# Optimization experiments

Hardware: AMD Instinct MI355X
Metric: run time of the kernel (lower is better)

Reference implementation:

```python
import jax, jax.numpy as jnp
import numpy as np
import math

N, M_KV = 8192, 8192
QDIM, KDIM, MID = 256, 256, 128
NEG_BIG = -float(1 << 32)  # matches torch.masked_fill(Attn, mask, -(1 << 32))


def setup_inputs() -> dict:
    key = jax.random.key(0)
    ks = jax.random.split(key, 8)
    main_feat = jax.random.normal(ks[0], (N, QDIM), dtype=jnp.float32)
    other_feat = jax.random.normal(ks[1], (M_KV, KDIM), dtype=jnp.float32)
    fix_feat = jax.random.uniform(ks[2], (M_KV,), dtype=jnp.float32)
    mask = jax.random.randint(ks[3], (N, M_KV), 0, 2).astype(jnp.bool_)
    # Linear params (torch.nn.Linear stores weight as [out, in])
    Wq = jax.random.normal(ks[4], (MID, QDIM), dtype=jnp.float32) / math.sqrt(QDIM)
    bq = jax.random.normal(ks[5], (MID,), dtype=jnp.float32) * 0.01
    Wk = jax.random.normal(ks[6], (MID, KDIM), dtype=jnp.float32) / math.sqrt(KDIM)
    bk = jax.random.normal(ks[7], (MID,), dtype=jnp.float32) * 0.01
    return {"main_feat": main_feat, "other_feat": other_feat, "fix_feat": fix_feat,
            "mask": mask, "Wq": Wq, "bq": bq, "Wk": Wk, "bk": bk}


def reference(main_feat, other_feat, fix_feat, mask, Wq, bq, Wk, bk):
    # Projections: y = x @ W.T + b
    Q = main_feat @ Wq.T + bq            # [N, MID]
    K = other_feat @ Wk.T + bk           # [M, MID]
    scale = 1.0 / math.sqrt(MID)
    attn = jnp.einsum('nd,md->nm', Q, K) * scale   # [N, M]
    attn = jnp.where(mask, NEG_BIG, attn)
    attn = jax.nn.softmax(attn, axis=-1)
    # diag(fix_feat) @ other_feat is just a row-wise scale of V
    V = fix_feat[:, None] * other_feat   # [M, KDIM]
    return attn @ V                      # [N, KDIM]
```

## Files before the change

kernel.cpp:

```cpp
#include <hip/hip_runtime.h>
#include <hip/hip_bf16.h>
#include <stdint.h>

typedef __attribute__((ext_vector_type(8))) short short8;
typedef __attribute__((ext_vector_type(4))) float floatx4;

#define MFMA32K(a, b, c) __builtin_amdgcn_mfma_f32_16x16x32_bf16(a, b, c, 0, 0, 0)

constexpr int N_Q  = 8192;
constexpr int M_KV = 8192;
constexpr int DMID = 128;
constexpr int DV   = 256;

__device__ __forceinline__ unsigned short f2bf(float x) {
    unsigned u = __float_as_uint(x);
    u += 0x7fffu + ((u >> 16) & 1u);
    return (unsigned short)(u >> 16);
}

__device__ __forceinline__ short8 cvt_f8_bf8(float4 a, float4 b) {
    short8 r;
    r[0] = (short)f2bf(a.x); r[1] = (short)f2bf(a.y);
    r[2] = (short)f2bf(a.z); r[3] = (short)f2bf(a.w);
    r[4] = (short)f2bf(b.x); r[5] = (short)f2bf(b.y);
    r[6] = (short)f2bf(b.z); r[7] = (short)f2bf(b.w);
    return r;
}

__device__ __forceinline__ void gl_lds16(const unsigned short* g, unsigned short* l) {
    __builtin_amdgcn_global_load_lds(
        (const __attribute__((address_space(1))) unsigned int*)g,
        (__attribute__((address_space(3))) unsigned int*)l, 16, 0, 0);
}

__device__ __forceinline__ unsigned nz4(unsigned x) {
    unsigned nz = (((x & 0x7f7f7f7fu) + 0x7f7f7f7fu) | x) & 0x80808080u;
    unsigned a = (nz >> 7) & 0x01010101u;
    return (a * 0x01020408u) >> 24;
}

__global__ __launch_bounds__(256) void proj_kernel(
    const float* __restrict__ main_feat, const float* __restrict__ Wq, const float* __restrict__ bq,
    const float* __restrict__ other_feat, const float* __restrict__ Wk, const float* __restrict__ bk,
    unsigned short* __restrict__ Qw, unsigned short* __restrict__ Kw)
{
    const float* src;  const float* W;  const float* bias;  unsigned short* dst;
    if (blockIdx.y == 0) { src = main_feat;  W = Wq; bias = bq; dst = Qw; }
    else                 { src = other_feat; W = Wk; bias = bk; dst = Kw; }

    const int wave = threadIdx.x >> 6, lane = threadIdx.x & 63;
    const int n = lane & 15, quad = lane >> 4;
    const int row0 = blockIdx.x * 64 + wave * 16;

    short8 a[8];
    const float* ap = src + (size_t)(row0 + n) * 256 + quad * 8;
#pragma unroll
    for (int ks = 0; ks < 8; ++ks) {
        float4 x0 = *(const float4*)(ap + ks * 32);
        float4 x1 = *(const float4*)(ap + ks * 32 + 4);
        a[ks] = cvt_f8_bf8(x0, x1);
    }

    floatx4 acc[8];
#pragma unroll
    for (int nt = 0; nt < 8; ++nt) acc[nt] = floatx4{0.f, 0.f, 0.f, 0.f};

#pragma unroll
    for (int nt = 0; nt < 8; ++nt) {
        const float* wp = W + (size_t)(nt * 16 + n) * 256 + quad * 8;
#pragma unroll
        for (int ks = 0; ks < 8; ++ks) {
            float4 w0 = *(const float4*)(wp + ks * 32);
            float4 w1 = *(const float4*)(wp + ks * 32 + 4);
            short8 b = cvt_f8_bf8(w0, w1);
            acc[nt] = MFMA32K(a[ks], b, acc[nt]);
        }
    }

#pragma unroll
    for (int nt = 0; nt < 8; ++nt) {
        float bb = bias[nt * 16 + n];
#pragma unroll
        for (int reg = 0; reg < 4; ++reg) {
            int r = row0 + quad * 4 + reg;
            int c = nt * 16 + n;
            int phys = ((((c >> 3) + r) & 15) << 3) | (c & 7);
            dst[(size_t)r * DMID + phys] = f2bf(acc[nt][reg] + bb);
        }
    }
}

__global__ __launch_bounds__(256) void build_vt_kernel(
    const float* __restrict__ other_feat, const float* __restrict__ fix_feat,
    unsigned short* __restrict__ Vt)
{
    __shared__ unsigned short tile[64 * 72];
    const int t = threadIdx.x;
    const int m0 = blockIdx.x * 64, d0 = blockIdx.y * 64;

#pragma unroll
    for (int r = 0; r < 4; ++r) {
        int idx = r * 256 + t;
        int ml = idx >> 4, dl4 = (idx & 15) * 4;
        float4 v = *(const float4*)(other_feat + (size_t)(m0 + ml) * 256 + d0 + dl4);
        float f = fix_feat[m0 + ml];
        tile[(dl4 + 0) * 72 + ml] = f2bf(v.x * f);
        tile[(dl4 + 1) * 72 + ml] = f2bf(v.y * f);
        tile[(dl4 + 2) * 72 + ml] = f2bf(v.z * f);
        tile[(dl4 + 3) * 72 + ml] = f2bf(v.w * f);
    }
    __syncthreads();
#pragma unroll
    for (int r = 0; r < 8; ++r) {
        int dl = r * 8 + (t >> 5);
        int d = d0 + dl;
        int ml = (t & 31) * 2;
        int e = ml >> 5, s = (ml >> 4) & 1, q = (ml >> 2) & 3, j = ml & 3;
        int pc = e * 32 + q * 8 + s * 4 + j;
        int phys = ((((pc >> 3) + d) & 7) << 3) | (pc & 7);
        unsigned int v0 = tile[dl * 72 + ml];
        unsigned int v1 = tile[dl * 72 + ml + 1];
        *(unsigned int*)(Vt + (size_t)d * M_KV + m0 + phys) = v0 | (v1 << 16);
    }
}

template<int ESZ>
__device__ __forceinline__ void flash_body(
    const unsigned short* __restrict__ Qw, const unsigned short* __restrict__ Kw,
    const unsigned short* __restrict__ Vt, const unsigned int* __restrict__ mask,
    unsigned short* __restrict__ Opart, float* __restrict__ Lpart,
    int nsplit, int lgNs,
    unsigned short* k_lds , unsigned short* vt_lds )
{
    const int L = blockIdx.x + gridDim.x * blockIdx.y;
    const int ly = L & (nsplit - 1);
    const int lx = L >> lgNs;
    const int chunkLen = M_KV >> lgNs;
    const int mBeg = ly * chunkLen;
    const int iters = chunkLen / 64;
    const int phase = lx & (iters - 1);
    const int tid = threadIdx.x;
    const int wave = tid >> 6, lane = tid & 63, n = lane & 15, quad = lane >> 4;
    const int qrow0 = lx * 128 + wave * 32;
    constexpr float SC = 0.08838834764831845f * 1.4426950408889634f;

    auto mcol = [&](int it) {
        int idx = it + phase;
        if (idx >= iters) idx -= iters;
        return mBeg + idx * 64;
    };

    short8 qf[2][4];
#pragma unroll
    for (int qt = 0; qt < 2; ++qt)
#pragma unroll
        for (int db = 0; db < 4; ++db) {
            int row = qrow0 + qt * 16 + n;
            int phys = (db * 4 + quad + row) & 15;
            qf[qt][db] = *(const short8*)(Qw + (size_t)row * DMID + phys * 8);
        }

    floatx4 Oacc[2][16];
#pragma unroll
    for (int qt = 0; qt < 2; ++qt)
#pragma unroll
        for (int dt = 0; dt < 16; ++dt) Oacc[qt][dt] = floatx4{0.f, 0.f, 0.f, 0.f};

    float lrow[2] = {0.f, 0.f};

    const unsigned short* kg = Kw + (size_t)(wave * 4 + (lane >> 4)) * DMID + (lane & 15) * 8;
    const unsigned short* vg = Vt + (size_t)(wave * 8 + (lane >> 3)) * M_KV + (lane & 7) * 8;
    unsigned short* vld = &vt_lds[wave * 512];
    const int kqn = quad + n;

    uint4    mv4[2][4];
    unsigned mv1[2][4];

    auto load_mask = [&](int m0l) {
#pragma unroll
        for (int qt = 0; qt < 2; ++qt) {
            const size_t row = (size_t)(qrow0 + qt * 16 + n);
            if constexpr (ESZ == 4) {
                const unsigned* mp = mask + row * M_KV + m0l + quad * 4;
#pragma unroll
                for (int kvt = 0; kvt < 4; ++kvt)
                    mv4[qt][kvt] = *(const uint4*)(mp + kvt * 16);
            } else {
                const unsigned* mp = mask + row * (M_KV / 4) + (m0l >> 2) + quad;
#pragma unroll
                for (int kvt = 0; kvt < 4; ++kvt)
                    mv1[qt][kvt] = mp[kvt * 4];
            }
        }
    };

    {
        const int m0p = mcol(0);
#pragma unroll
        for (int r = 0; r < 4; ++r)
            gl_lds16(kg + (size_t)(m0p + r * 16) * DMID, &k_lds[wave * 512 + r * 2048]);
        load_mask(m0p);
    }

    for (int it = 0; it < iters; ++it) {
        const int m0 = mcol(it);
        const unsigned short* kbuf = k_lds + (it & 1) * 8192;

        __syncthreads();

#pragma unroll
        for (int r = 0; r < 8; ++r)
            gl_lds16(vg + (size_t)(r * 32) * M_KV + m0, vld + r * 2048);

        unsigned wq[2];
#pragma unroll
        for (int qt = 0; qt < 2; ++qt) {
            unsigned b = 0;
            if constexpr (ESZ == 4) {
#pragma unroll
                for (int kvt = 0; kvt < 4; ++kvt) {
                    const unsigned* c = (const unsigned*)&mv4[qt][kvt];
#pragma unroll
                    for (int j = 0; j < 4; ++j)
                        b |= (c[j] != 0u ? 1u : 0u) << (kvt * 4 + j);
                }
            } else {
#pragma unroll
                for (int kvt = 0; kvt < 4; ++kvt)
                    b |= nz4(mv1[qt][kvt]) << (kvt * 4);
            }
            wq[qt] = b;
        }

        floatx4 ST[4][2];
        __builtin_amdgcn_s_setprio(1);
#pragma unroll
        for (int kvt = 0; kvt < 4; ++kvt) {
            const int rowoff = (kvt * 16 + n) * DMID;
            short8 a0 = *(const short8*)&kbuf[rowoff + (((kqn + 0) & 15) << 3)];
            short8 a1 = *(const short8*)&kbuf[rowoff + (((kqn + 4) & 15) << 3)];
            short8 a2 = *(const short8*)&kbuf[rowoff + (((kqn + 8) & 15) << 3)];
            short8 a3 = *(const short8*)&kbuf[rowoff + (((kqn + 12) & 15) << 3)];
#pragma unroll
            for (int qt = 0; qt < 2; ++qt) {
                floatx4 s = floatx4{0.f, 0.f, 0.f, 0.f};
                s = MFMA32K(a0, qf[qt][0], s);
                s = MFMA32K(a1, qf[qt][1], s);
                s = MFMA32K(a2, qf[qt][2], s);
                s = MFMA32K(a3, qf[qt][3], s);
                ST[kvt][qt] = s;
            }
        }
        __builtin_amdgcn_s_setprio(0);

        short8 pf8[2][2];
#pragma unroll
        for (int qt = 0; qt < 2; ++qt) {
            const unsigned x = wq[qt];
            float lacc = 0.f;
#pragma unroll
            for (int kvt = 0; kvt < 4; ++kvt) {
                int e = kvt >> 1, s = kvt & 1;
                float p[4];
#pragma unroll
                for (int j = 0; j < 4; ++j) {
                    float v = __builtin_amdgcn_exp2f(ST[kvt][qt][j] * SC);
                    p[j] = ((x >> (kvt * 4 + j)) & 1u) ? 0.f : v;
                    lacc += p[j];
                }
                __hip_bfloat162 h0 = __float22bfloat162_rn(make_float2(p[0], p[1]));
                __hip_bfloat162 h1 = __float22bfloat162_rn(make_float2(p[2], p[3]));
                unsigned u0, u1;
                __builtin_memcpy(&u0, &h0, 4);
                __builtin_memcpy(&u1, &h1, 4);
                ((unsigned*)&pf8[qt][e])[s * 2 + 0] = u0;
                ((unsigned*)&pf8[qt][e])[s * 2 + 1] = u1;
            }
            lrow[qt] += lacc;
        }

        __syncthreads();

        if (it + 1 < iters) {
            const int m1 = mcol(it + 1);
            unsigned short* knext = k_lds + ((it + 1) & 1) * 8192 + wave * 512;
#pragma unroll
            for (int r = 0; r < 4; ++r)
                gl_lds16(kg + (size_t)(m1 + r * 16) * DMID, knext + r * 2048);
            load_mask(m1);
        }

        __builtin_amdgcn_s_setprio(1);
#pragma unroll
        for (int e = 0; e < 2; ++e) {
#pragma unroll
            for (int dt = 0; dt < 16; ++dt) {
                const int vb = (dt * 16 + n) * 64 + (((e * 4 + quad + n) & 7) << 3);
                short8 bv = *(const short8*)&vt_lds[vb];
                Oacc[0][dt] = MFMA32K(pf8[0][e], bv, Oacc[0][dt]);
                Oacc[1][dt] = MFMA32K(pf8[1][e], bv, Oacc[1][dt]);
            }
        }
        __builtin_amdgcn_s_setprio(0);
    }

    const size_t obase = (size_t)ly * N_Q * DV;
#pragma unroll
    for (int qt = 0; qt < 2; ++qt)
#pragma unroll
        for (int dt = 0; dt < 16; ++dt)
#pragma unroll
            for (int reg = 0; reg < 4; ++reg) {
                int gr = qrow0 + qt * 16 + quad * 4 + reg;
                Opart[obase + (size_t)gr * DV + dt * 16 + n] = f2bf(Oacc[qt][dt][reg]);
            }
#pragma unroll
    for (int qt = 0; qt < 2; ++qt) {
        float r = lrow[qt];
        r += __shfl_xor(r, 16);
        r += __shfl_xor(r, 32);
        if (quad == 0)
            Lpart[ly * N_Q + qrow0 + qt * 16 + n] = r;
    }
}

__global__ __launch_bounds__(256, 2) void flash_kernel(
    const unsigned short* __restrict__ Qw, const unsigned short* __restrict__ Kw,
    const unsigned short* __restrict__ Vt, const unsigned int* __restrict__ mask,
    unsigned short* __restrict__ Opart, float* __restrict__ Lpart,
    int nsplit, int lgNs)
{
    __shared__ __align__(16) unsigned short k_lds[2][64 * 128];
    __shared__ __align__(16) unsigned short vt_lds[256 * 64];

    unsigned w0 = mask[threadIdx.x & 63];
    bool isf = (w0 == 0x3f800000u);
    bool isb = (w0 > 1u) && !isf;
    bool wide = (__ballot(isf) != 0ull) || (__ballot(isb) == 0ull);

    if (wide)
        flash_body<4>(Qw, Kw, Vt, mask, Opart, Lpart, nsplit, lgNs,
                      &k_lds[0][0], vt_lds);
    else
        flash_body<1>(Qw, Kw, Vt, mask, Opart, Lpart, nsplit, lgNs,
                      &k_lds[0][0], vt_lds);
}

__global__ __launch_bounds__(256) void combine_kernel(
    const unsigned short* __restrict__ Opart, const float* __restrict__ Lpart,
    float* __restrict__ out, int nsplit)
{
    const int row = blockIdx.x, d = threadIdx.x;
    float L = 0.f, o = 0.f;
    for (int c = 0; c < nsplit; ++c) {
        L += Lpart[c * N_Q + row];
        unsigned int b = Opart[((size_t)c * N_Q + row) * DV + d];
        o += __uint_as_float(b << 16);
    }
    out[(size_t)row * DV + d] = o / L;
}

extern "C" void kernel_launch(void* const* d_in, const int* in_sizes, int n_in,
                              void* d_out, int out_size, void* d_ws, size_t ws_size,
                              hipStream_t stream)
{
    const float* main_feat  = (const float*)d_in[0];
    const float* other_feat = (const float*)d_in[1];
    const float* fix_feat   = (const float*)d_in[2];
    const void*  mask       = d_in[3];
    const float* Wq         = (const float*)d_in[4];
    const float* bq         = (const float*)d_in[5];
    const float* Wk         = (const float*)d_in[6];
    const float* bk         = (const float*)d_in[7];
    float* out = (float*)d_out;

    char* ws = (char*)d_ws;
    unsigned short* Qw = (unsigned short*)(ws);
    unsigned short* Kw = (unsigned short*)(ws + (1ull << 21));
    unsigned short* Vt = (unsigned short*)(ws + (2ull << 21));
    float* Lpart = (float*)(ws + (16ull << 20) + 2048);

    const size_t base = (16ull << 20) + 2048;
    auto need = [&](int ns) {
        return base + (size_t)ns * N_Q * 4 + (size_t)ns * N_Q * DV * 2;
    };
    int nsplit = 1, lgNs = 0;
    if (ws_size >= need(8))      { nsplit = 8; lgNs = 3; }
    else if (ws_size >= need(4)) { nsplit = 4; lgNs = 2; }
    else if (ws_size >= need(2)) { nsplit = 2; lgNs = 1; }

    unsigned short* Opart = (unsigned short*)(Lpart + (size_t)nsplit * N_Q);

    hipLaunchKernelGGL(proj_kernel, dim3(128, 2), dim3(256), 0, stream,
                       main_feat, Wq, bq, other_feat, Wk, bk, Qw, Kw);
    hipLaunchKernelGGL(build_vt_kernel, dim3(128, 4), dim3(256), 0, stream,
                       other_feat, fix_feat, Vt);
    hipLaunchKernelGGL(flash_kernel, dim3(64, nsplit), dim3(256), 0, stream,
                       Qw, Kw, Vt, (const unsigned int*)mask, Opart, Lpart, nsplit, lgNs);
    hipLaunchKernelGGL(combine_kernel, dim3(N_Q), dim3(256), 0, stream,
                       Opart, Lpart, out, nsplit);
}
```

Baseline: 459.9 us.

## Drop LDS staging of K and V; read MFMA operands directly from global memory

Removes the shared-memory double buffer for K and the V tile. Each wave now loads its K and Vt MFMA fragments straight from global memory (through L2/L1), which eliminates both block-wide barriers per iteration and frees LDS. In exchange, every wave in the block redundantly fetches the same K/V data, and the loads are no longer prefetched ahead of the compute, so the MFMAs may stall on global-memory latency.

```diff
diff --git a/kernel.cpp b/kernel.cpp
--- a/kernel.cpp
+++ b/kernel.cpp
@@ -25,12 +25,6 @@
     r[4] = (short)f2bf(b.x); r[5] = (short)f2bf(b.y);
     r[6] = (short)f2bf(b.z); r[7] = (short)f2bf(b.w);
     return r;
-}
-
-__device__ __forceinline__ void gl_lds16(const unsigned short* g, unsigned short* l) {
-    __builtin_amdgcn_global_load_lds(
-        (const __attribute__((address_space(1))) unsigned int*)g,
-        (__attribute__((address_space(3))) unsigned int*)l, 16, 0, 0);
 }
 
 __device__ __forceinline__ unsigned nz4(unsigned x) {
@@ -129,8 +123,7 @@
     const unsigned short* __restrict__ Qw, const unsigned short* __restrict__ Kw,
     const unsigned short* __restrict__ Vt, const unsigned int* __restrict__ mask,
     unsigned short* __restrict__ Opart, float* __restrict__ Lpart,
-    int nsplit, int lgNs,
-    unsigned short* k_lds , unsigned short* vt_lds )
+    int nsplit, int lgNs)
 {
     const int L = blockIdx.x + gridDim.x * blockIdx.y;
     const int ly = L & (nsplit - 1);
@@ -168,9 +161,6 @@
 
     float lrow[2] = {0.f, 0.f};
 
-    const unsigned short* kg = Kw + (size_t)(wave * 4 + (lane >> 4)) * DMID + (lane & 15) * 8;
-    const unsigned short* vg = Vt + (size_t)(wave * 8 + (lane >> 3)) * M_KV + (lane & 7) * 8;
-    unsigned short* vld = &vt_lds[wave * 512];
     const int kqn = quad + n;
 
     uint4    mv4[2][4];
@@ -194,23 +184,10 @@
         }
     };
 
-    {
-        const int m0p = mcol(0);
-#pragma unroll
-        for (int r = 0; r < 4; ++r)
-            gl_lds16(kg + (size_t)(m0p + r * 16) * DMID, &k_lds[wave * 512 + r * 2048]);
-        load_mask(m0p);
-    }
+    load_mask(mcol(0));
 
     for (int it = 0; it < iters; ++it) {
         const int m0 = mcol(it);
-        const unsigned short* kbuf = k_lds + (it & 1) * 8192;
-
-        __syncthreads();
-
-#pragma unroll
-        for (int r = 0; r < 8; ++r)
-            gl_lds16(vg + (size_t)(r * 32) * M_KV + m0, vld + r * 2048);
 
         unsigned wq[2];
 #pragma unroll
@@ -236,11 +213,11 @@
         __builtin_amdgcn_s_setprio(1);
 #pragma unroll
         for (int kvt = 0; kvt < 4; ++kvt) {
-            const int rowoff = (kvt * 16 + n) * DMID;
-            short8 a0 = *(const short8*)&kbuf[rowoff + (((kqn + 0) & 15) << 3)];
-            short8 a1 = *(const short8*)&kbuf[rowoff + (((kqn + 4) & 15) << 3)];
-            short8 a2 = *(const short8*)&kbuf[rowoff + (((kqn + 8) & 15) << 3)];
-            short8 a3 = *(const short8*)&kbuf[rowoff + (((kqn + 12) & 15) << 3)];
+            const unsigned short* krow = Kw + (size_t)(m0 + kvt * 16 + n) * DMID;
+            short8 a0 = *(const short8*)(krow + (((kqn + 0) & 15) << 3));
+            short8 a1 = *(const short8*)(krow + (((kqn + 4) & 15) << 3));
+            short8 a2 = *(const short8*)(krow + (((kqn + 8) & 15) << 3));
+            short8 a3 = *(const short8*)(krow + (((kqn + 12) & 15) << 3));
 #pragma unroll
             for (int qt = 0; qt < 2; ++qt) {
                 floatx4 s = floatx4{0.f, 0.f, 0.f, 0.f};
@@ -279,24 +256,15 @@
             lrow[qt] += lacc;
         }
 
-        __syncthreads();
-
-        if (it + 1 < iters) {
-            const int m1 = mcol(it + 1);
-            unsigned short* knext = k_lds + ((it + 1) & 1) * 8192 + wave * 512;
-#pragma unroll
-            for (int r = 0; r < 4; ++r)
-                gl_lds16(kg + (size_t)(m1 + r * 16) * DMID, knext + r * 2048);
-            load_mask(m1);
-        }
+        if (it + 1 < iters) load_mask(mcol(it + 1));
 
         __builtin_amdgcn_s_setprio(1);
 #pragma unroll
         for (int e = 0; e < 2; ++e) {
 #pragma unroll
             for (int dt = 0; dt < 16; ++dt) {
-                const int vb = (dt * 16 + n) * 64 + (((e * 4 + quad + n) & 7) << 3);
-                short8 bv = *(const short8*)&vt_lds[vb];
+                const unsigned short* vrow = Vt + (size_t)(dt * 16 + n) * M_KV + m0;
+                short8 bv = *(const short8*)(vrow + (((e * 4 + quad + n) & 7) << 3));
                 Oacc[0][dt] = MFMA32K(pf8[0][e], bv, Oacc[0][dt]);
                 Oacc[1][dt] = MFMA32K(pf8[1][e], bv, Oacc[1][dt]);
             }
@@ -330,20 +298,15 @@
     unsigned short* __restrict__ Opart, float* __restrict__ Lpart,
     int nsplit, int lgNs)
 {
-    __shared__ __align__(16) unsigned short k_lds[2][64 * 128];
-    __shared__ __align__(16) unsigned short vt_lds[256 * 64];
-
     unsigned w0 = mask[threadIdx.x & 63];
     bool isf = (w0 == 0x3f800000u);
     bool isb = (w0 > 1u) && !isf;
     bool wide = (__ballot(isf) != 0ull) || (__ballot(isb) == 0ull);
 
     if (wide)
-        flash_body<4>(Qw, Kw, Vt, mask, Opart, Lpart, nsplit, lgNs,
-                      &k_lds[0][0], vt_lds);
+        flash_body<4>(Qw, Kw, Vt, mask, Opart, Lpart, nsplit, lgNs);
     else
-        flash_body<1>(Qw, Kw, Vt, mask, Opart, Lpart, nsplit, lgNs,
-                      &k_lds[0][0], vt_lds);
+        flash_body<1>(Qw, Kw, Vt, mask, Opart, Lpart, nsplit, lgNs);
 }
 
 __global__ __launch_bounds__(256) void combine_kernel(
```

Measured after the change: 621.5 us. 1.35x slower.

## Use 8 waves of 16 query rows each with manual waitcnt/barrier pipelining

Applied to the files above, without the earlier changes.

The flash kernel now runs 512 threads per block, with each wave owning one 16-row query tile instead of two, which halves per-wave accumulators and register pressure. The launch bounds go to (512,4) to target higher occupancy. K, V and mask loads are reissued earlier in each iteration, and __syncthreads is replaced by explicit s_waitcnt vmcnt/lgkmcnt plus s_barrier with sched_barriers, so memory traffic overlaps compute. In exchange each K/V tile in LDS is reused by fewer query rows per wave, the block carries more barrier traffic, and the hand-tuned vmcnt counts must match the number of outstanding loads.

```diff
diff --git a/kernel.cpp b/kernel.cpp
--- a/kernel.cpp
+++ b/kernel.cpp
@@ -141,7 +141,7 @@
     const int phase = lx & (iters - 1);
     const int tid = threadIdx.x;
     const int wave = tid >> 6, lane = tid & 63, n = lane & 15, quad = lane >> 4;
-    const int qrow0 = lx * 128 + wave * 32;
+    const int qrow0 = lx * 128 + wave * 16;
     constexpr float SC = 0.08838834764831845f * 1.4426950408889634f;
 
     auto mcol = [&](int it) {
@@ -150,89 +150,87 @@
         return mBeg + idx * 64;
     };
 
-    short8 qf[2][4];
-#pragma unroll
-    for (int qt = 0; qt < 2; ++qt)
-#pragma unroll
-        for (int db = 0; db < 4; ++db) {
-            int row = qrow0 + qt * 16 + n;
-            int phys = (db * 4 + quad + row) & 15;
-            qf[qt][db] = *(const short8*)(Qw + (size_t)row * DMID + phys * 8);
-        }
-
-    floatx4 Oacc[2][16];
-#pragma unroll
-    for (int qt = 0; qt < 2; ++qt)
-#pragma unroll
-        for (int dt = 0; dt < 16; ++dt) Oacc[qt][dt] = floatx4{0.f, 0.f, 0.f, 0.f};
-
-    float lrow[2] = {0.f, 0.f};
+    short8 qf[4];
+#pragma unroll
+    for (int db = 0; db < 4; ++db) {
+        int row = qrow0 + n;
+        int phys = (db * 4 + quad + row) & 15;
+        qf[db] = *(const short8*)(Qw + (size_t)row * DMID + phys * 8);
+    }
+
+    floatx4 Oacc[16];
+#pragma unroll
+    for (int dt = 0; dt < 16; ++dt) Oacc[dt] = floatx4{0.f, 0.f, 0.f, 0.f};
+
+    float lrow = 0.f;
 
     const unsigned short* kg = Kw + (size_t)(wave * 4 + (lane >> 4)) * DMID + (lane & 15) * 8;
     const unsigned short* vg = Vt + (size_t)(wave * 8 + (lane >> 3)) * M_KV + (lane & 7) * 8;
-    unsigned short* vld = &vt_lds[wave * 512];
     const int kqn = quad + n;
 
-    uint4    mv4[2][4];
-    unsigned mv1[2][4];
+    uint4    mv4[4];
+    unsigned mv1[4];
 
     auto load_mask = [&](int m0l) {
-#pragma unroll
-        for (int qt = 0; qt < 2; ++qt) {
-            const size_t row = (size_t)(qrow0 + qt * 16 + n);
-            if constexpr (ESZ == 4) {
-                const unsigned* mp = mask + row * M_KV + m0l + quad * 4;
-#pragma unroll
-                for (int kvt = 0; kvt < 4; ++kvt)
-                    mv4[qt][kvt] = *(const uint4*)(mp + kvt * 16);
-            } else {
-                const unsigned* mp = mask + row * (M_KV / 4) + (m0l >> 2) + quad;
-#pragma unroll
-                for (int kvt = 0; kvt < 4; ++kvt)
-                    mv1[qt][kvt] = mp[kvt * 4];
-            }
+        const size_t row = (size_t)(qrow0 + n);
+        if constexpr (ESZ == 4) {
+            const unsigned* mp = mask + row * M_KV + m0l + quad * 4;
+#pragma unroll
+            for (int kvt = 0; kvt < 4; ++kvt)
+                mv4[kvt] = *(const uint4*)(mp + kvt * 16);
+        } else {
+            const unsigned* mp = mask + row * (M_KV / 4) + (m0l >> 2) + quad;
+#pragma unroll
+            for (int kvt = 0; kvt < 4; ++kvt)
+                mv1[kvt] = mp[kvt * 4];
         }
     };
 
-    {
-        const int m0p = mcol(0);
-#pragma unroll
-        for (int r = 0; r < 4; ++r)
-            gl_lds16(kg + (size_t)(m0p + r * 16) * DMID, &k_lds[wave * 512 + r * 2048]);
-        load_mask(m0p);
-    }
+#pragma unroll
+    for (int r = 0; r < 2; ++r)
+        gl_lds16(kg + (size_t)(mcol(0) + r * 32) * DMID, &k_lds[wave * 512 + r * 4096]);
+    __builtin_amdgcn_sched_barrier(0);
+    load_mask(mcol(0));
+    __builtin_amdgcn_sched_barrier(0);
+    asm volatile("s_waitcnt vmcnt(4)\n\ts_barrier" ::: "memory");
 
     for (int it = 0; it < iters; ++it) {
         const int m0 = mcol(it);
         const unsigned short* kbuf = k_lds + (it & 1) * 8192;
 
-        __syncthreads();
-
-#pragma unroll
-        for (int r = 0; r < 8; ++r)
-            gl_lds16(vg + (size_t)(r * 32) * M_KV + m0, vld + r * 2048);
-
-        unsigned wq[2];
-#pragma unroll
-        for (int qt = 0; qt < 2; ++qt) {
-            unsigned b = 0;
-            if constexpr (ESZ == 4) {
-#pragma unroll
-                for (int kvt = 0; kvt < 4; ++kvt) {
-                    const unsigned* c = (const unsigned*)&mv4[qt][kvt];
-#pragma unroll
-                    for (int j = 0; j < 4; ++j)
-                        b |= (c[j] != 0u ? 1u : 0u) << (kvt * 4 + j);
-                }
-            } else {
-#pragma unroll
-                for (int kvt = 0; kvt < 4; ++kvt)
-                    b |= nz4(mv1[qt][kvt]) << (kvt * 4);
+#pragma unroll
+        for (int r = 0; r < 4; ++r)
+            gl_lds16(vg + (size_t)(r * 64) * M_KV + m0, &vt_lds[wave * 512 + r * 4096]);
+        const bool more = (it + 1 < iters);
+        if (more) {
+            const int m1 = mcol(it + 1);
+            unsigned short* knext = k_lds + ((it + 1) & 1) * 8192 + wave * 512;
+#pragma unroll
+            for (int r = 0; r < 2; ++r)
+                gl_lds16(kg + (size_t)(m1 + r * 32) * DMID, knext + r * 4096);
+        }
+        __builtin_amdgcn_sched_barrier(0);
+
+        unsigned wq = 0;
+        if constexpr (ESZ == 4) {
+#pragma unroll
+            for (int kvt = 0; kvt < 4; ++kvt) {
+                const unsigned* c = (const unsigned*)&mv4[kvt];
+#pragma unroll
+                for (int j = 0; j < 4; ++j)
+                    wq |= (c[j] != 0u ? 1u : 0u) << (kvt * 4 + j);
             }
-            wq[qt] = b;
-        }
-
-        floatx4 ST[4][2];
+        } else {
+#pragma unroll
+            for (int kvt = 0; kvt < 4; ++kvt)
+                wq |= nz4(mv1[kvt]) << (kvt * 4);
+        }
+        __builtin_amdgcn_sched_barrier(0);
+
+        if (more) load_mask(mcol(it + 1));
+        __builtin_amdgcn_sched_barrier(0);
+
+        floatx4 ST[4];
         __builtin_amdgcn_s_setprio(1);
 #pragma unroll
         for (int kvt = 0; kvt < 4; ++kvt) {
@@ -241,54 +239,39 @@
             short8 a1 = *(const short8*)&kbuf[rowoff + (((kqn + 4) & 15) << 3)];
             short8 a2 = *(const short8*)&kbuf[rowoff + (((kqn + 8) & 15) << 3)];
             short8 a3 = *(const short8*)&kbuf[rowoff + (((kqn + 12) & 15) << 3)];
-#pragma unroll
-            for (int qt = 0; qt < 2; ++qt) {
-                floatx4 s = floatx4{0.f, 0.f, 0.f, 0.f};
-                s = MFMA32K(a0, qf[qt][0], s);
-                s = MFMA32K(a1, qf[qt][1], s);
-                s = MFMA32K(a2, qf[qt][2], s);
-                s = MFMA32K(a3, qf[qt][3], s);
-                ST[kvt][qt] = s;
+            floatx4 s = floatx4{0.f, 0.f, 0.f, 0.f};
+            s = MFMA32K(a0, qf[0], s);
+            s = MFMA32K(a1, qf[1], s);
+            s = MFMA32K(a2, qf[2], s);
+            s = MFMA32K(a3, qf[3], s);
+            ST[kvt] = s;
+        }
+        __builtin_amdgcn_s_setprio(0);
+
+        short8 pf8[2];
+#pragma unroll
+        for (int kvt = 0; kvt < 4; ++kvt) {
+            int e = kvt >> 1, s = kvt & 1;
+            float p[4];
+#pragma unroll
+            for (int j = 0; j < 4; ++j) {
+                float v = __builtin_amdgcn_exp2f(ST[kvt][j] * SC);
+                p[j] = ((wq >> (kvt * 4 + j)) & 1u) ? 0.f : v;
+                lrow += p[j];
             }
-        }
-        __builtin_amdgcn_s_setprio(0);
-
-        short8 pf8[2][2];
-#pragma unroll
-        for (int qt = 0; qt < 2; ++qt) {
-            const unsigned x = wq[qt];
-            float lacc = 0.f;
-#pragma unroll
-            for (int kvt = 0; kvt < 4; ++kvt) {
-                int e = kvt >> 1, s = kvt & 1;
-                float p[4];
-#pragma unroll
-                for (int j = 0; j < 4; ++j) {
-                    float v = __builtin_amdgcn_exp2f(ST[kvt][qt][j] * SC);
-                    p[j] = ((x >> (kvt * 4 + j)) & 1u) ? 0.f : v;
-                    lacc += p[j];
-                }
-                __hip_bfloat162 h0 = __float22bfloat162_rn(make_float2(p[0], p[1]));
-                __hip_bfloat162 h1 = __float22bfloat162_rn(make_float2(p[2], p[3]));
-                unsigned u0, u1;
-                __builtin_memcpy(&u0, &h0, 4);
-                __builtin_memcpy(&u1, &h1, 4);
-                ((unsigned*)&pf8[qt][e])[s * 2 + 0] = u0;
-                ((unsigned*)&pf8[qt][e])[s * 2 + 1] = u1;
-            }
-            lrow[qt] += lacc;
-        }
-
-        __syncthreads();
-
-        if (it + 1 < iters) {
-            const int m1 = mcol(it + 1);
-            unsigned short* knext = k_lds + ((it + 1) & 1) * 8192 + wave * 512;
-#pragma unroll
-            for (int r = 0; r < 4; ++r)
-                gl_lds16(kg + (size_t)(m1 + r * 16) * DMID, knext + r * 2048);
-            load_mask(m1);
-        }
+            __hip_bfloat162 h0 = __float22bfloat162_rn(make_float2(p[0], p[1]));
+            __hip_bfloat162 h1 = __float22bfloat162_rn(make_float2(p[2], p[3]));
+            unsigned u0, u1;
+            __builtin_memcpy(&u0, &h0, 4);
+            __builtin_memcpy(&u1, &h1, 4);
+            ((unsigned*)&pf8[e])[s * 2 + 0] = u0;
+            ((unsigned*)&pf8[e])[s * 2 + 1] = u1;
+        }
+
+        if (more)
+            asm volatile("s_waitcnt vmcnt(4) lgkmcnt(0)\n\ts_barrier" ::: "memory");
+        else
+            asm volatile("s_waitcnt vmcnt(0) lgkmcnt(0)\n\ts_barrier" ::: "memory");
 
         __builtin_amdgcn_s_setprio(1);
 #pragma unroll
@@ -297,34 +280,32 @@
             for (int dt = 0; dt < 16; ++dt) {
                 const int vb = (dt * 16 + n) * 64 + (((e * 4 + quad + n) & 7) << 3);
                 short8 bv = *(const short8*)&vt_lds[vb];
-                Oacc[0][dt] = MFMA32K(pf8[0][e], bv, Oacc[0][dt]);
-                Oacc[1][dt] = MFMA32K(pf8[1][e], bv, Oacc[1][dt]);
+                Oacc[dt] = MFMA32K(pf8[e], bv, Oacc[dt]);
             }
         }
         __builtin_amdgcn_s_setprio(0);
+
+        asm volatile("s_waitcnt lgkmcnt(0)\n\ts_barrier" ::: "memory");
     }
 
     const size_t obase = (size_t)ly * N_Q * DV;
 #pragma unroll
-    for (int qt = 0; qt < 2; ++qt)
-#pragma unroll
-        for (int dt = 0; dt < 16; ++dt)
-#pragma unroll
-            for (int reg = 0; reg < 4; ++reg) {
-                int gr = qrow0 + qt * 16 + quad * 4 + reg;
-                Opart[obase + (size_t)gr * DV + dt * 16 + n] = f2bf(Oacc[qt][dt][reg]);
-            }
-#pragma unroll
-    for (int qt = 0; qt < 2; ++qt) {
-        float r = lrow[qt];
+    for (int dt = 0; dt < 16; ++dt)
+#pragma unroll
+        for (int reg = 0; reg < 4; ++reg) {
+            int gr = qrow0 + quad * 4 + reg;
+            Opart[obase + (size_t)gr * DV + dt * 16 + n] = f2bf(Oacc[dt][reg]);
+        }
+    {
+        float r = lrow;
         r += __shfl_xor(r, 16);
         r += __shfl_xor(r, 32);
         if (quad == 0)
-            Lpart[ly * N_Q + qrow0 + qt * 16 + n] = r;
-    }
-}
-
-__global__ __launch_bounds__(256, 2) void flash_kernel(
+            Lpart[ly * N_Q + qrow0 + n] = r;
+    }
+}
+
+__global__ __launch_bounds__(512, 4) void flash_kernel(
     const unsigned short* __restrict__ Qw, const unsigned short* __restrict__ Kw,
     const unsigned short* __restrict__ Vt, const unsigned int* __restrict__ mask,
     unsigned short* __restrict__ Opart, float* __restrict__ Lpart,
@@ -395,7 +376,7 @@
                        main_feat, Wq, bq, other_feat, Wk, bk, Qw, Kw);
     hipLaunchKernelGGL(build_vt_kernel, dim3(128, 4), dim3(256), 0, stream,
                        other_feat, fix_feat, Vt);
-    hipLaunchKernelGGL(flash_kernel, dim3(64, nsplit), dim3(256), 0, stream,
+    hipLaunchKernelGGL(flash_kernel, dim3(64, nsplit), dim3(512), 0, stream,
                        Qw, Kw, Vt, (const unsigned int*)mask, Opart, Lpart, nsplit, lgNs);
     hipLaunchKernelGGL(combine_kernel, dim3(N_Q), dim3(256), 0, stream,
                        Opart, Lpart, out, nsplit);
```

Result: slower. 535.2 us (+16.4%).
